# Kernel optimization log

Measured on AMD Instinct MI355X. Metric: run time of the kernel, lower is better.

## Reference

```python
import jax, jax.numpy as jnp
import numpy as np

TOP_K = 2

def setup_inputs() -> dict:
    key = jax.random.key(0)
    k0, k1, k2, k3, k4 = jax.random.split(key, 5)
    B, S, D, H, E = 2, 2048, 1024, 2048, 8
    x = jax.random.normal(k0, (B, S, D), dtype=jnp.float32)
    router_w = jax.random.normal(k1, (D, E), dtype=jnp.float32) * (1.0 / np.sqrt(D))
    wg = jax.random.normal(k2, (E, D, H), dtype=jnp.float32) * (1.0 / np.sqrt(D))
    wu = jax.random.normal(k3, (E, D, H), dtype=jnp.float32) * (1.0 / np.sqrt(D))
    wd = jax.random.normal(k4, (E, H, D), dtype=jnp.float32) * (1.0 / np.sqrt(H))
    return {"x": x, "router_w": router_w, "wg": wg, "wu": wu, "wd": wd}

def reference(x, router_w, wg, wu, wd):
    B, S, D = x.shape
    E = router_w.shape[1]
    xf = x.reshape(-1, D)                                   # [T, D]
    router_logits = xf @ router_w                           # [T, E]
    top_logits, top_idx = jax.lax.top_k(router_logits, TOP_K)
    top_w = jax.nn.softmax(top_logits, axis=-1)             # [T, k]
    # Dense combine weights: W[t, e] = routing weight if e in top-k of t, else 0.
    combine = jnp.sum(jax.nn.one_hot(top_idx, E, dtype=x.dtype) * top_w[..., None], axis=1)  # [T, E]
    # SwiGLU experts, computed for all tokens and masked by the combine weights
    # (mathematically identical to the gather/scatter form in the original).
    gate = jnp.einsum('td,edh->eth', xf, wg)                # [E, T, H]
    up = jnp.einsum('td,edh->eth', xf, wu)                  # [E, T, H]
    fused = jax.nn.silu(gate) * up                          # [E, T, H]
    expert_out = jnp.einsum('eth,ehd->etd', fused, wd)      # [E, T, D]
    y = jnp.einsum('etd,te->td', expert_out, combine)       # [T, D]
    return y.reshape(B, S, D)
```

## Files before the change

kernel.cpp:

```cpp
#include <hip/hip_runtime.h>
#include <hip/hip_bf16.h>

#define T_TOK 4096
#define DDIM  1024
#define HDIM  2048
#define NEXP  8
#define MAXSLOT 9216

typedef __attribute__((ext_vector_type(4))) float f32x4;
typedef __attribute__((ext_vector_type(8))) short s16x8;
typedef __hip_bfloat16 bf16;

typedef const void __attribute__((address_space(1))) gvoid;
typedef void __attribute__((address_space(3))) svoid;

__device__ __forceinline__ void gload16(const void* g, void* l) {
    __builtin_amdgcn_global_load_lds((gvoid*)g, (svoid*)l, 16, 0, 0);
}

__device__ __forceinline__ int frag_off(int rr, int kq) {
    int lr = rr >> 1;
    int ch = ((rr & 1) << 2) + (kq >> 3);
    return lr * 64 + (ch ^ (lr & 7)) * 8;
}

__global__ void router_cast_kernel(const float* __restrict__ x, const float* __restrict__ rw,
                                   int* __restrict__ r_e, float* __restrict__ r_w,
                                   bf16* __restrict__ xb) {
    int wave = threadIdx.x >> 6, lane = threadIdx.x & 63;
    int t = blockIdx.x * 4 + wave;
    const float* xr = x + (size_t)t * DDIM;
    bf16* xbr = xb + (size_t)t * DDIM;
    double acc[NEXP];
#pragma unroll
    for (int e = 0; e < NEXP; ++e) acc[e] = 0.0;
#pragma unroll
    for (int c = 0; c < 4; ++c) {
        int d = c * 256 + lane * 4;
        float4 v = *reinterpret_cast<const float4*>(xr + d);
        union { ushort4 u; bf16 h[4]; } o;
        o.h[0] = __float2bfloat16(v.x);
        o.h[1] = __float2bfloat16(v.y);
        o.h[2] = __float2bfloat16(v.z);
        o.h[3] = __float2bfloat16(v.w);
        *reinterpret_cast<ushort4*>(xbr + d) = o.u;
        const float* rw0 = rw + (size_t)d * NEXP;
#pragma unroll
        for (int j = 0; j < 4; ++j) {
            float xv = (&v.x)[j];
            const float* rwr = rw0 + j * NEXP;
#pragma unroll
            for (int e = 0; e < NEXP; ++e) acc[e] += (double)xv * (double)rwr[e];
        }
    }
#pragma unroll
    for (int e = 0; e < NEXP; ++e) {
#pragma unroll
        for (int off = 32; off > 0; off >>= 1) acc[e] += __shfl_down(acc[e], off);
    }
    if (lane == 0) {
        int i0 = 0; double v0 = acc[0];
#pragma unroll
        for (int e = 1; e < NEXP; ++e) if (acc[e] > v0) { v0 = acc[e]; i0 = e; }
        int i1 = -1; double v1 = -1e300;
#pragma unroll
        for (int e = 0; e < NEXP; ++e) { if (e == i0) continue; if (acc[e] > v1) { v1 = acc[e]; i1 = e; } }
        float w0 = 1.0f / (1.0f + expf((float)(v1 - v0)));
        float w1 = 1.0f - w0;
        r_e[2*t]   = i0; r_e[2*t+1] = i1;
        r_w[2*t]   = w0; r_w[2*t+1] = w1;
    }
}

__global__ void binning_kernel(const int* __restrict__ r_e, const float* __restrict__ r_w,
                               int* __restrict__ offs, int* __restrict__ cnt,
                               int* __restrict__ list, float* __restrict__ slot_w) {
    __shared__ int scnt[NEXP], scur[NEXP], soff[NEXP + 1];
    int tid = threadIdx.x;
    if (tid < NEXP) { scnt[tid] = 0; scur[tid] = 0; }
    __syncthreads();
    for (int i = tid; i < 2 * T_TOK; i += 512) atomicAdd(&scnt[r_e[i]], 1);
    __syncthreads();
    if (tid == 0) {
        int s = 0;
        for (int e = 0; e < NEXP; ++e) { soff[e] = s; s += (scnt[e] + 127) & ~127; }
        soff[NEXP] = s;
    }
    __syncthreads();
    if (tid < NEXP + 1) offs[tid] = soff[tid];
    if (tid < NEXP) cnt[tid] = scnt[tid];
    for (int i = tid; i < 2 * T_TOK; i += 512) {
        int e = r_e[i];
        int pos = atomicAdd(&scur[e], 1);
        int slot = soff[e] + pos;
        list[slot] = i >> 1;
        slot_w[slot] = r_w[i];
    }
}

__global__ void transpose_gu_kernel(const float* __restrict__ wg, const float* __restrict__ wu,
                                    bf16* __restrict__ wguT) {
    __shared__ bf16 tile[64][68];
    int which = blockIdx.z >> 3;
    int e = blockIdx.z & 7;
    const float* inp = (which ? wu : wg) + (size_t)e * DDIM * HDIM;
    bf16* outp = wguT + (size_t)e * 2 * HDIM * DDIM;
    int r0 = blockIdx.x * 64, c0 = blockIdx.y * 64;
    int tid = threadIdx.x;
#pragma unroll
    for (int i = 0; i < 4; ++i) {
        int idx = i * 256 + tid;
        int r = idx >> 4, c4 = (idx & 15) * 4;
        float4 v = *reinterpret_cast<const float4*>(inp + (size_t)(r0 + r) * HDIM + c0 + c4);
        union { ushort4 u; bf16 h[4]; } o;
        o.h[0] = __float2bfloat16(v.x);
        o.h[1] = __float2bfloat16(v.y);
        o.h[2] = __float2bfloat16(v.z);
        o.h[3] = __float2bfloat16(v.w);
        *reinterpret_cast<ushort4*>(&tile[r][c4]) = o.u;
    }
    __syncthreads();
#pragma unroll
    for (int i = 0; i < 4; ++i) {
        int idx = i * 256 + tid;
        int c = idx >> 4, r4 = (idx & 15) * 4;
        union { ushort4 u; bf16 h[4]; } w;
        w.h[0] = tile[r4 + 0][c];
        w.h[1] = tile[r4 + 1][c];
        w.h[2] = tile[r4 + 2][c];
        w.h[3] = tile[r4 + 3][c];
        *reinterpret_cast<ushort4*>(outp + ((size_t)(c0 + c) * 2 + which) * DDIM + r0 + r4) = w.u;
    }
}

__global__ void transpose_wd_kernel(const float* __restrict__ wd, bf16* __restrict__ wdT) {
    __shared__ bf16 tile[64][68];
    const float* inp = wd + (size_t)blockIdx.z * HDIM * DDIM;
    bf16* outp = wdT + (size_t)blockIdx.z * DDIM * HDIM;
    int r0 = blockIdx.x * 64, c0 = blockIdx.y * 64;
    int tid = threadIdx.x;
#pragma unroll
    for (int i = 0; i < 4; ++i) {
        int idx = i * 256 + tid;
        int r = idx >> 4, c4 = (idx & 15) * 4;
        float4 v = *reinterpret_cast<const float4*>(inp + (size_t)(r0 + r) * DDIM + c0 + c4);
        union { ushort4 u; bf16 h[4]; } o;
        o.h[0] = __float2bfloat16(v.x);
        o.h[1] = __float2bfloat16(v.y);
        o.h[2] = __float2bfloat16(v.z);
        o.h[3] = __float2bfloat16(v.w);
        *reinterpret_cast<ushort4*>(&tile[r][c4]) = o.u;
    }
    __syncthreads();
#pragma unroll
    for (int i = 0; i < 4; ++i) {
        int idx = i * 256 + tid;
        int c = idx >> 4, r4 = (idx & 15) * 4;
        union { ushort4 u; bf16 h[4]; } w;
        w.h[0] = tile[r4 + 0][c];
        w.h[1] = tile[r4 + 1][c];
        w.h[2] = tile[r4 + 2][c];
        w.h[3] = tile[r4 + 3][c];
        *reinterpret_cast<ushort4*>(outp + (size_t)(c0 + c) * HDIM + r0 + r4) = w.u;
    }
}

__device__ __forceinline__ int find_expert(const int* offs, int slot0) {
    int e = 0;
#pragma unroll
    for (int i = 0; i < NEXP - 1; ++i) e += (offs[e + 1] <= slot0) ? 1 : 0;
    return e;
}

__global__ __launch_bounds__(256, 2)
void gateup_kernel(const bf16* __restrict__ xb, const bf16* __restrict__ wguT,
                   const int* __restrict__ offs, const int* __restrict__ cnt,
                   const int* __restrict__ list, bf16* __restrict__ hbuf) {
    int slot0 = blockIdx.y * 128;
    if (slot0 >= offs[NEXP]) return;
    int e = find_expert(offs, slot0);
    int base = offs[e];
    int ne = cnt[e];
    int m0 = slot0 - base;
    int n0 = blockIdx.x * 128;

    __shared__ bf16 As[3][4096];
    __shared__ bf16 Bs[3][4096];

    int tid = threadIdx.x, lane = tid & 63, wid = tid >> 6;

    const bf16* bbase = wguT + (size_t)e * (2 * HDIM) * DDIM + (size_t)n0 * DDIM;

    const bf16* aS[2]; const bf16* bS[2];
    int sdst[2];
#pragma unroll
    for (int j = 0; j < 2; ++j) {
        int q = wid + j * 4;
        int lr = q * 8 + (lane >> 3);
        int ch = (lane & 7) ^ (lr & 7);
        int rr = 2 * lr + (ch >> 2);
        int koff = (ch & 3) * 8;
        int r = m0 + rr; if (r > ne - 1) r = ne - 1;
        aS[j] = xb + (size_t)list[base + r] * DDIM + koff;
        bS[j] = bbase + (size_t)rr * DDIM + koff;
        sdst[j] = q * 512;
    }

    int rl = lane & 15, kq = 8 * (lane >> 4);
    int wrow = (wid >> 1) * 64;
    int wcol = (wid & 1) * 64;
    int offA[4], offB[4];
#pragma unroll
    for (int mi = 0; mi < 4; ++mi) offA[mi] = frag_off(wrow + mi * 16 + rl, kq);
#pragma unroll
    for (int ni = 0; ni < 4; ++ni) offB[ni] = frag_off(wcol + ni * 16 + rl, kq);

    f32x4 zero4 = {0.f, 0.f, 0.f, 0.f};
    f32x4 acc[4][4];
#pragma unroll
    for (int mi = 0; mi < 4; ++mi)
#pragma unroll
        for (int ni = 0; ni < 4; ++ni) acc[mi][ni] = zero4;

    const int nk = DDIM / 32;

#define GU_STAGE(tt, buf)                                     \
    {                                                         \
        int k0 = (tt) * 32;                                   \
        gload16(aS[0] + k0, &As[buf][sdst[0]]);               \
        gload16(aS[1] + k0, &As[buf][sdst[1]]);               \
        gload16(bS[0] + k0, &Bs[buf][sdst[0]]);               \
        gload16(bS[1] + k0, &Bs[buf][sdst[1]]);               \
    }

    GU_STAGE(0, 0);
    GU_STAGE(1, 1);
    asm volatile("s_waitcnt vmcnt(4)" ::: "memory");
    __builtin_amdgcn_s_barrier();

    int cb = 0;
    for (int t = 0; t < nk; ++t) {
        int sb = cb + 2; if (sb >= 3) sb -= 3;
        if (t + 2 < nk) GU_STAGE(t + 2, sb);
        const bf16* Ab = As[cb];
        const bf16* Bb = Bs[cb];
        s16x8 a[4], b[4];
#pragma unroll
        for (int mi = 0; mi < 4; ++mi) a[mi] = *reinterpret_cast<const s16x8*>(Ab + offA[mi]);
#pragma unroll
        for (int ni = 0; ni < 4; ++ni) b[ni] = *reinterpret_cast<const s16x8*>(Bb + offB[ni]);
        __builtin_amdgcn_s_setprio(1);
#pragma unroll
        for (int mi = 0; mi < 4; ++mi)
#pragma unroll
            for (int ni = 0; ni < 4; ++ni)
                acc[mi][ni] = __builtin_amdgcn_mfma_f32_16x16x32_bf16(a[mi], b[ni], acc[mi][ni], 0, 0, 0);
        __builtin_amdgcn_s_setprio(0);
        __builtin_amdgcn_sched_barrier(0);
        if (t + 1 < nk) {
            if (t + 2 < nk) asm volatile("s_waitcnt vmcnt(4)" ::: "memory");
            else            asm volatile("s_waitcnt vmcnt(0)" ::: "memory");
            __builtin_amdgcn_s_barrier();
        }
        cb = cb + 1; if (cb >= 3) cb -= 3;
    }
#undef GU_STAGE

    int rbase = (lane >> 4) * 4, cbase = lane & 15;
    bool evenlane = (lane & 1) == 0;
#pragma unroll
    for (int mi = 0; mi < 4; ++mi) {
#pragma unroll
        for (int ni = 0; ni < 4; ++ni) {
#pragma unroll
            for (int r = 0; r < 4; ++r) {
                float own = acc[mi][ni][r];
                float oth = __shfl_xor(own, 1);
                int row = m0 + wrow + mi * 16 + rbase + r;
                if (evenlane && row < ne) {
                    float g = own, u = oth;
                    float h = (g / (1.0f + expf(-g))) * u;
                    int hcol = (n0 + wcol + ni * 16 + cbase) >> 1;
                    hbuf[(size_t)(base + row) * HDIM + hcol] = __float2bfloat16(h);
                }
            }
        }
    }
}

__global__ __launch_bounds__(256, 2)
void down_kernel(const bf16* __restrict__ hbuf, const bf16* __restrict__ wdT,
                 const int* __restrict__ offs, const int* __restrict__ cnt,
                 const int* __restrict__ list, const float* __restrict__ slot_w,
                 float* __restrict__ y) {
    int slot0 = blockIdx.y * 128;
    if (slot0 >= offs[NEXP]) return;
    int e = find_expert(offs, slot0);
    int base = offs[e];
    int ne = cnt[e];
    int m0 = slot0 - base;
    int n0 = blockIdx.x * 128;

    __shared__ bf16 As[3][4096];
    __shared__ bf16 Bs[3][4096];

    int tid = threadIdx.x, lane = tid & 63, wid = tid >> 6;

    const bf16* bbase = wdT + (size_t)e * DDIM * HDIM + (size_t)n0 * HDIM;

    const bf16* aS[2]; const bf16* bS[2];
    int sdst[2];
#pragma unroll
    for (int j = 0; j < 2; ++j) {
        int q = wid + j * 4;
        int lr = q * 8 + (lane >> 3);
        int ch = (lane & 7) ^ (lr & 7);
        int rr = 2 * lr + (ch >> 2);
        int koff = (ch & 3) * 8;
        int r = m0 + rr; if (r > ne - 1) r = ne - 1;
        aS[j] = hbuf + (size_t)(base + r) * HDIM + koff;
        bS[j] = bbase + (size_t)rr * HDIM + koff;
        sdst[j] = q * 512;
    }

    int rl = lane & 15, kq = 8 * (lane >> 4);
    int wrow = (wid >> 1) * 64;
    int wcol = (wid & 1) * 64;
    int offA[4], offB[4];
#pragma unroll
    for (int mi = 0; mi < 4; ++mi) offA[mi] = frag_off(wrow + mi * 16 + rl, kq);
#pragma unroll
    for (int ni = 0; ni < 4; ++ni) offB[ni] = frag_off(wcol + ni * 16 + rl, kq);

    f32x4 zero4 = {0.f, 0.f, 0.f, 0.f};
    f32x4 acc[4][4];
#pragma unroll
    for (int mi = 0; mi < 4; ++mi)
#pragma unroll
        for (int ni = 0; ni < 4; ++ni) acc[mi][ni] = zero4;

    const int nk = HDIM / 32;

#define DN_STAGE(tt, buf)                                     \
    {                                                         \
        int k0 = (tt) * 32;                                   \
        gload16(aS[0] + k0, &As[buf][sdst[0]]);               \
        gload16(aS[1] + k0, &As[buf][sdst[1]]);               \
        gload16(bS[0] + k0, &Bs[buf][sdst[0]]);               \
        gload16(bS[1] + k0, &Bs[buf][sdst[1]]);               \
    }

    DN_STAGE(0, 0);
    DN_STAGE(1, 1);
    asm volatile("s_waitcnt vmcnt(4)" ::: "memory");
    __builtin_amdgcn_s_barrier();

    int cb = 0;
    for (int t = 0; t < nk; ++t) {
        int sb = cb + 2; if (sb >= 3) sb -= 3;
        if (t + 2 < nk) DN_STAGE(t + 2, sb);
        const bf16* Ab = As[cb];
        const bf16* Bb = Bs[cb];
        s16x8 a[4], b[4];
#pragma unroll
        for (int mi = 0; mi < 4; ++mi) a[mi] = *reinterpret_cast<const s16x8*>(Ab + offA[mi]);
#pragma unroll
        for (int ni = 0; ni < 4; ++ni) b[ni] = *reinterpret_cast<const s16x8*>(Bb + offB[ni]);
        __builtin_amdgcn_s_setprio(1);
#pragma unroll
        for (int mi = 0; mi < 4; ++mi)
#pragma unroll
            for (int ni = 0; ni < 4; ++ni)
                acc[mi][ni] = __builtin_amdgcn_mfma_f32_16x16x32_bf16(a[mi], b[ni], acc[mi][ni], 0, 0, 0);
        __builtin_amdgcn_s_setprio(0);
        __builtin_amdgcn_sched_barrier(0);
        if (t + 1 < nk) {
            if (t + 2 < nk) asm volatile("s_waitcnt vmcnt(4)" ::: "memory");
            else            asm volatile("s_waitcnt vmcnt(0)" ::: "memory");
            __builtin_amdgcn_s_barrier();
        }
        cb = cb + 1; if (cb >= 3) cb -= 3;
    }
#undef DN_STAGE

    int rbase = (lane >> 4) * 4, cbase = lane & 15;
#pragma unroll
    for (int mi = 0; mi < 4; ++mi) {
#pragma unroll
        for (int r = 0; r < 4; ++r) {
            int row = m0 + wrow + mi * 16 + rbase + r;
            if (row < ne) {
                int slot = base + row;
                int tok = list[slot];
                float w = slot_w[slot];
                float* yrow = y + (size_t)tok * DDIM + n0 + wcol + cbase;
#pragma unroll
                for (int ni = 0; ni < 4; ++ni)
                    atomicAdd(yrow + ni * 16, w * acc[mi][ni][r]);
            }
        }
    }
}

extern "C" void kernel_launch(void* const* d_in, const int* in_sizes, int n_in,
                              void* d_out, int out_size, void* d_ws, size_t ws_size,
                              hipStream_t stream) {
    const float* x  = (const float*)d_in[0];
    const float* rw = (const float*)d_in[1];
    const float* wg = (const float*)d_in[2];
    const float* wu = (const float*)d_in[3];
    const float* wd = (const float*)d_in[4];
    float* y = (float*)d_out;

    char* ws = (char*)d_ws;
    int*   r_e    = (int*)  (ws + 0);
    float* r_w    = (float*)(ws + 32768);
    int*   offs   = (int*)  (ws + 65600);
    int*   cnt    = (int*)  (ws + 65640);
    int*   list   = (int*)  (ws + 65792);
    float* slot_w = (float*)(ws + 65792 + 4 * MAXSLOT);
    bf16*  xb     = (bf16*) (ws + 1048576ull);
    bf16*  wguT   = (bf16*) (ws + 16777216ull);
    bf16*  wdT    = (bf16*) (ws + 83886080ull);
    bf16*  hbuf   = (bf16*) (ws + 117440512ull);

    transpose_gu_kernel<<<dim3(DDIM / 64, HDIM / 64, 2 * NEXP), 256, 0, stream>>>(wg, wu, wguT);
    transpose_wd_kernel<<<dim3(HDIM / 64, DDIM / 64, NEXP), 256, 0, stream>>>(wd, wdT);

    router_cast_kernel<<<dim3(T_TOK / 4), 256, 0, stream>>>(x, rw, r_e, r_w, xb);
    binning_kernel<<<dim3(1), 512, 0, stream>>>(r_e, r_w, offs, cnt, list, slot_w);

    hipMemsetAsync(d_out, 0, (size_t)out_size * sizeof(float), stream);

    gateup_kernel<<<dim3(2 * HDIM / 128, MAXSLOT / 128, 1), 256, 0, stream>>>(
        xb, wguT, offs, cnt, list, hbuf);
    down_kernel<<<dim3(DDIM / 128, MAXSLOT / 128, 1), 256, 0, stream>>>(
        hbuf, wdT, offs, cnt, list, slot_w, y);
}
```

Baseline: 286.2 us.

## Widen GEMM tiles to 128x256 with 512 threads and double buffering

Both grouped GEMM kernels move from 128x128 tiles with 4 waves to 128x256 tiles with 8 waves per block. Each A tile is now reused across twice as many output columns, and the block count along N is halved. The three-stage LDS pipeline is cut to two stages with a full vmcnt(0) wait every iteration, so each global load has less time to hide behind compute. LDS per block stays about the same at 48KB.

Measured after the change: 288.8 us. Within noise of the previous version (+0.9%).

```diff
diff --git a/kernel.cpp b/kernel.cpp
--- a/kernel.cpp
+++ b/kernel.cpp
@@ -172,7 +172,7 @@
     return e;
 }
 
-__global__ __launch_bounds__(256, 2)
+__global__ __launch_bounds__(512, 2)
 void gateup_kernel(const bf16* __restrict__ xb, const bf16* __restrict__ wguT,
                    const int* __restrict__ offs, const int* __restrict__ cnt,
                    const int* __restrict__ list, bf16* __restrict__ hbuf) {
@@ -182,33 +182,41 @@
     int base = offs[e];
     int ne = cnt[e];
     int m0 = slot0 - base;
-    int n0 = blockIdx.x * 128;
-
-    __shared__ bf16 As[3][4096];
-    __shared__ bf16 Bs[3][4096];
+    int n0 = blockIdx.x * 256;
+
+    __shared__ bf16 As[2][4096];
+    __shared__ bf16 Bs[2][8192];
 
     int tid = threadIdx.x, lane = tid & 63, wid = tid >> 6;
 
     const bf16* bbase = wguT + (size_t)e * (2 * HDIM) * DDIM + (size_t)n0 * DDIM;
 
-    const bf16* aS[2]; const bf16* bS[2];
-    int sdst[2];
-#pragma unroll
-    for (int j = 0; j < 2; ++j) {
-        int q = wid + j * 4;
+    const bf16* aS; const bf16* bS[2];
+    int sdstA, sdstB[2];
+    {
+        int q = wid;
         int lr = q * 8 + (lane >> 3);
         int ch = (lane & 7) ^ (lr & 7);
         int rr = 2 * lr + (ch >> 2);
         int koff = (ch & 3) * 8;
         int r = m0 + rr; if (r > ne - 1) r = ne - 1;
-        aS[j] = xb + (size_t)list[base + r] * DDIM + koff;
+        aS = xb + (size_t)list[base + r] * DDIM + koff;
+        sdstA = q * 512;
+    }
+#pragma unroll
+    for (int j = 0; j < 2; ++j) {
+        int q = wid + j * 8;
+        int lr = q * 8 + (lane >> 3);
+        int ch = (lane & 7) ^ (lr & 7);
+        int rr = 2 * lr + (ch >> 2);
+        int koff = (ch & 3) * 8;
         bS[j] = bbase + (size_t)rr * DDIM + koff;
-        sdst[j] = q * 512;
+        sdstB[j] = q * 512;
     }
 
     int rl = lane & 15, kq = 8 * (lane >> 4);
-    int wrow = (wid >> 1) * 64;
-    int wcol = (wid & 1) * 64;
+    int wrow = (wid >> 2) * 64;
+    int wcol = (wid & 3) * 64;
     int offA[4], offB[4];
 #pragma unroll
     for (int mi = 0; mi < 4; ++mi) offA[mi] = frag_off(wrow + mi * 16 + rl, kq);
@@ -227,23 +235,20 @@
 #define GU_STAGE(tt, buf)                                     \
     {                                                         \
         int k0 = (tt) * 32;                                   \
-        gload16(aS[0] + k0, &As[buf][sdst[0]]);               \
-        gload16(aS[1] + k0, &As[buf][sdst[1]]);               \
-        gload16(bS[0] + k0, &Bs[buf][sdst[0]]);               \
-        gload16(bS[1] + k0, &Bs[buf][sdst[1]]);               \
+        gload16(aS + k0, &As[buf][sdstA]);                    \
+        gload16(bS[0] + k0, &Bs[buf][sdstB[0]]);              \
+        gload16(bS[1] + k0, &Bs[buf][sdstB[1]]);              \
     }
 
     GU_STAGE(0, 0);
-    GU_STAGE(1, 1);
-    asm volatile("s_waitcnt vmcnt(4)" ::: "memory");
+    asm volatile("s_waitcnt vmcnt(0)" ::: "memory");
     __builtin_amdgcn_s_barrier();
 
-    int cb = 0;
+    int cur = 0;
     for (int t = 0; t < nk; ++t) {
-        int sb = cb + 2; if (sb >= 3) sb -= 3;
-        if (t + 2 < nk) GU_STAGE(t + 2, sb);
-        const bf16* Ab = As[cb];
-        const bf16* Bb = Bs[cb];
+        if (t + 1 < nk) GU_STAGE(t + 1, cur ^ 1);
+        const bf16* Ab = As[cur];
+        const bf16* Bb = Bs[cur];
         s16x8 a[4], b[4];
 #pragma unroll
         for (int mi = 0; mi < 4; ++mi) a[mi] = *reinterpret_cast<const s16x8*>(Ab + offA[mi]);
@@ -258,11 +263,10 @@
         __builtin_amdgcn_s_setprio(0);
         __builtin_amdgcn_sched_barrier(0);
         if (t + 1 < nk) {
-            if (t + 2 < nk) asm volatile("s_waitcnt vmcnt(4)" ::: "memory");
-            else            asm volatile("s_waitcnt vmcnt(0)" ::: "memory");
+            asm volatile("s_waitcnt vmcnt(0)" ::: "memory");
             __builtin_amdgcn_s_barrier();
         }
-        cb = cb + 1; if (cb >= 3) cb -= 3;
+        cur ^= 1;
     }
 #undef GU_STAGE
 
@@ -288,7 +292,7 @@
     }
 }
 
-__global__ __launch_bounds__(256, 2)
+__global__ __launch_bounds__(512, 2)
 void down_kernel(const bf16* __restrict__ hbuf, const bf16* __restrict__ wdT,
                  const int* __restrict__ offs, const int* __restrict__ cnt,
                  const int* __restrict__ list, const float* __restrict__ slot_w,
@@ -299,33 +303,41 @@
     int base = offs[e];
     int ne = cnt[e];
     int m0 = slot0 - base;
-    int n0 = blockIdx.x * 128;
-
-    __shared__ bf16 As[3][4096];
-    __shared__ bf16 Bs[3][4096];
+    int n0 = blockIdx.x * 256;
+
+    __shared__ bf16 As[2][4096];
+    __shared__ bf16 Bs[2][8192];
 
     int tid = threadIdx.x, lane = tid & 63, wid = tid >> 6;
 
     const bf16* bbase = wdT + (size_t)e * DDIM * HDIM + (size_t)n0 * HDIM;
 
-    const bf16* aS[2]; const bf16* bS[2];
-    int sdst[2];
-#pragma unroll
-    for (int j = 0; j < 2; ++j) {
-        int q = wid + j * 4;
+    const bf16* aS; const bf16* bS[2];
+    int sdstA, sdstB[2];
+    {
+        int q = wid;
         int lr = q * 8 + (lane >> 3);
         int ch = (lane & 7) ^ (lr & 7);
         int rr = 2 * lr + (ch >> 2);
         int koff = (ch & 3) * 8;
         int r = m0 + rr; if (r > ne - 1) r = ne - 1;
-        aS[j] = hbuf + (size_t)(base + r) * HDIM + koff;
+        aS = hbuf + (size_t)(base + r) * HDIM + koff;
+        sdstA = q * 512;
+    }
+#pragma unroll
+    for (int j = 0; j < 2; ++j) {
+        int q = wid + j * 8;
+        int lr = q * 8 + (lane >> 3);
+        int ch = (lane & 7) ^ (lr & 7);
+        int rr = 2 * lr + (ch >> 2);
+        int koff = (ch & 3) * 8;
         bS[j] = bbase + (size_t)rr * HDIM + koff;
-        sdst[j] = q * 512;
+        sdstB[j] = q * 512;
     }
 
     int rl = lane & 15, kq = 8 * (lane >> 4);
-    int wrow = (wid >> 1) * 64;
-    int wcol = (wid & 1) * 64;
+    int wrow = (wid >> 2) * 64;
+    int wcol = (wid & 3) * 64;
     int offA[4], offB[4];
 #pragma unroll
     for (int mi = 0; mi < 4; ++mi) offA[mi] = frag_off(wrow + mi * 16 + rl, kq);
@@ -344,23 +356,20 @@
 #define DN_STAGE(tt, buf)                                     \
     {                                                         \
         int k0 = (tt) * 32;                                   \
-        gload16(aS[0] + k0, &As[buf][sdst[0]]);               \
-        gload16(aS[1] + k0, &As[buf][sdst[1]]);               \
-        gload16(bS[0] + k0, &Bs[buf][sdst[0]]);               \
-        gload16(bS[1] + k0, &Bs[buf][sdst[1]]);               \
+        gload16(aS + k0, &As[buf][sdstA]);                    \
+        gload16(bS[0] + k0, &Bs[buf][sdstB[0]]);              \
+        gload16(bS[1] + k0, &Bs[buf][sdstB[1]]);              \
     }
 
     DN_STAGE(0, 0);
-    DN_STAGE(1, 1);
-    asm volatile("s_waitcnt vmcnt(4)" ::: "memory");
+    asm volatile("s_waitcnt vmcnt(0)" ::: "memory");
     __builtin_amdgcn_s_barrier();
 
-    int cb = 0;
+    int cur = 0;
     for (int t = 0; t < nk; ++t) {
-        int sb = cb + 2; if (sb >= 3) sb -= 3;
-        if (t + 2 < nk) DN_STAGE(t + 2, sb);
-        const bf16* Ab = As[cb];
-        const bf16* Bb = Bs[cb];
+        if (t + 1 < nk) DN_STAGE(t + 1, cur ^ 1);
+        const bf16* Ab = As[cur];
+        const bf16* Bb = Bs[cur];
         s16x8 a[4], b[4];
 #pragma unroll
         for (int mi = 0; mi < 4; ++mi) a[mi] = *reinterpret_cast<const s16x8*>(Ab + offA[mi]);
@@ -375,11 +384,10 @@
         __builtin_amdgcn_s_setprio(0);
         __builtin_amdgcn_sched_barrier(0);
         if (t + 1 < nk) {
-            if (t + 2 < nk) asm volatile("s_waitcnt vmcnt(4)" ::: "memory");
-            else            asm volatile("s_waitcnt vmcnt(0)" ::: "memory");
+            asm volatile("s_waitcnt vmcnt(0)" ::: "memory");
             __builtin_amdgcn_s_barrier();
         }
-        cb = cb + 1; if (cb >= 3) cb -= 3;
+        cur ^= 1;
     }
 #undef DN_STAGE
 
@@ -432,8 +440,8 @@
 
     hipMemsetAsync(d_out, 0, (size_t)out_size * sizeof(float), stream);
 
-    gateup_kernel<<<dim3(2 * HDIM / 128, MAXSLOT / 128, 1), 256, 0, stream>>>(
+    gateup_kernel<<<dim3(2 * HDIM / 256, MAXSLOT / 128, 1), 512, 0, stream>>>(
         xb, wguT, offs, cnt, list, hbuf);
-    down_kernel<<<dim3(DDIM / 128, MAXSLOT / 128, 1), 256, 0, stream>>>(
+    down_kernel<<<dim3(DDIM / 256, MAXSLOT / 128, 1), 512, 0, stream>>>(
         hbuf, wdT, offs, cnt, list, slot_w, y);
 }
```

## Use 512-thread blocks with BK=64 double-buffered tiles in expert GEMMs

Applied to the files above, without the earlier changes.

Both the gate/up and down expert GEMM kernels move from 256 threads with a 3-stage BK=32 pipeline to 512 threads (8 waves, each owning a 64x32 sub-tile) with a 2-stage BK=64 double buffer. The LDS layout becomes a simple 64-wide row with XOR swizzle, and the number of k-iterations and barriers per tile is halved. The aim is more waves to hide latency and less loop and sync overhead per k-step. In exchange, each wave does half the MFMAs per fragment load, so it gets less register reuse, and prefetch depth drops to one stage with an extra barrier per iteration.

Result: no change. 284.1 us (-0.7%).

```diff
diff --git a/kernel.cpp b/kernel.cpp
--- a/kernel.cpp
+++ b/kernel.cpp
@@ -16,12 +16,6 @@
 
 __device__ __forceinline__ void gload16(const void* g, void* l) {
     __builtin_amdgcn_global_load_lds((gvoid*)g, (svoid*)l, 16, 0, 0);
-}
-
-__device__ __forceinline__ int frag_off(int rr, int kq) {
-    int lr = rr >> 1;
-    int ch = ((rr & 1) << 2) + (kq >> 3);
-    return lr * 64 + (ch ^ (lr & 7)) * 8;
 }
 
 __global__ void router_cast_kernel(const float* __restrict__ x, const float* __restrict__ rw,
@@ -172,7 +166,7 @@
     return e;
 }
 
-__global__ __launch_bounds__(256, 2)
+__global__ __launch_bounds__(512, 2)
 void gateup_kernel(const bf16* __restrict__ xb, const bf16* __restrict__ wguT,
                    const int* __restrict__ offs, const int* __restrict__ cnt,
                    const int* __restrict__ list, bf16* __restrict__ hbuf) {
@@ -184,10 +178,12 @@
     int m0 = slot0 - base;
     int n0 = blockIdx.x * 128;
 
-    __shared__ bf16 As[3][4096];
-    __shared__ bf16 Bs[3][4096];
+    __shared__ bf16 As[2][8192];
+    __shared__ bf16 Bs[2][8192];
 
     int tid = threadIdx.x, lane = tid & 63, wid = tid >> 6;
+    int sub = lane >> 3;
+    int koff = 8 * ((lane & 7) ^ sub);
 
     const bf16* bbase = wguT + (size_t)e * (2 * HDIM) * DDIM + (size_t)n0 * DDIM;
 
@@ -195,75 +191,68 @@
     int sdst[2];
 #pragma unroll
     for (int j = 0; j < 2; ++j) {
-        int q = wid + j * 4;
-        int lr = q * 8 + (lane >> 3);
-        int ch = (lane & 7) ^ (lr & 7);
-        int rr = 2 * lr + (ch >> 2);
-        int koff = (ch & 3) * 8;
-        int r = m0 + rr; if (r > ne - 1) r = ne - 1;
+        int q = wid + j * 8;
+        int row = q * 8 + sub;
+        int r = m0 + row; if (r > ne - 1) r = ne - 1;
         aS[j] = xb + (size_t)list[base + r] * DDIM + koff;
-        bS[j] = bbase + (size_t)rr * DDIM + koff;
+        bS[j] = bbase + (size_t)row * DDIM + koff;
         sdst[j] = q * 512;
     }
 
     int rl = lane & 15, kq = 8 * (lane >> 4);
-    int wrow = (wid >> 1) * 64;
-    int wcol = (wid & 1) * 64;
-    int offA[4], offB[4];
-#pragma unroll
-    for (int mi = 0; mi < 4; ++mi) offA[mi] = frag_off(wrow + mi * 16 + rl, kq);
-#pragma unroll
-    for (int ni = 0; ni < 4; ++ni) offB[ni] = frag_off(wcol + ni * 16 + rl, kq);
+    int wrow = (wid >> 2) * 64;
+    int wcol = (wid & 3) * 32;
+    int xorv = (rl & 7) * 8;
 
     f32x4 zero4 = {0.f, 0.f, 0.f, 0.f};
-    f32x4 acc[4][4];
-#pragma unroll
-    for (int mi = 0; mi < 4; ++mi)
-#pragma unroll
-        for (int ni = 0; ni < 4; ++ni) acc[mi][ni] = zero4;
-
-    const int nk = DDIM / 32;
+    f32x4 acc[4][2];
+#pragma unroll
+    for (int mi = 0; mi < 4; ++mi) { acc[mi][0] = zero4; acc[mi][1] = zero4; }
+
+    const int nk = DDIM / 64;
 
 #define GU_STAGE(tt, buf)                                     \
     {                                                         \
-        int k0 = (tt) * 32;                                   \
+        int k0 = (tt) * 64;                                   \
         gload16(aS[0] + k0, &As[buf][sdst[0]]);               \
         gload16(aS[1] + k0, &As[buf][sdst[1]]);               \
         gload16(bS[0] + k0, &Bs[buf][sdst[0]]);               \
         gload16(bS[1] + k0, &Bs[buf][sdst[1]]);               \
     }
 
+#define GU_COMPUTE(Ab, Bb)                                                        \
+    _Pragma("unroll")                                                             \
+    for (int kk = 0; kk < 2; ++kk) {                                              \
+        int kos = (kk * 32 + kq) ^ xorv;                                          \
+        s16x8 a[4], b[2];                                                         \
+        _Pragma("unroll")                                                         \
+        for (int mi = 0; mi < 4; ++mi)                                            \
+            a[mi] = *reinterpret_cast<const s16x8*>(&(Ab)[(wrow + mi * 16 + rl) * 64 + kos]); \
+        _Pragma("unroll")                                                         \
+        for (int ni = 0; ni < 2; ++ni)                                            \
+            b[ni] = *reinterpret_cast<const s16x8*>(&(Bb)[(wcol + ni * 16 + rl) * 64 + kos]); \
+        __builtin_amdgcn_s_setprio(1);                                            \
+        _Pragma("unroll")                                                         \
+        for (int mi = 0; mi < 4; ++mi)                                            \
+            _Pragma("unroll")                                                     \
+            for (int ni = 0; ni < 2; ++ni)                                        \
+                acc[mi][ni] = __builtin_amdgcn_mfma_f32_16x16x32_bf16(a[mi], b[ni], acc[mi][ni], 0, 0, 0); \
+        __builtin_amdgcn_s_setprio(0);                                            \
+    }
+
     GU_STAGE(0, 0);
     GU_STAGE(1, 1);
-    asm volatile("s_waitcnt vmcnt(4)" ::: "memory");
-    __builtin_amdgcn_s_barrier();
-
-    int cb = 0;
+
     for (int t = 0; t < nk; ++t) {
-        int sb = cb + 2; if (sb >= 3) sb -= 3;
-        if (t + 2 < nk) GU_STAGE(t + 2, sb);
-        const bf16* Ab = As[cb];
-        const bf16* Bb = Bs[cb];
-        s16x8 a[4], b[4];
-#pragma unroll
-        for (int mi = 0; mi < 4; ++mi) a[mi] = *reinterpret_cast<const s16x8*>(Ab + offA[mi]);
-#pragma unroll
-        for (int ni = 0; ni < 4; ++ni) b[ni] = *reinterpret_cast<const s16x8*>(Bb + offB[ni]);
-        __builtin_amdgcn_s_setprio(1);
-#pragma unroll
-        for (int mi = 0; mi < 4; ++mi)
-#pragma unroll
-            for (int ni = 0; ni < 4; ++ni)
-                acc[mi][ni] = __builtin_amdgcn_mfma_f32_16x16x32_bf16(a[mi], b[ni], acc[mi][ni], 0, 0, 0);
-        __builtin_amdgcn_s_setprio(0);
+        if (t + 1 < nk) asm volatile("s_waitcnt vmcnt(4)" ::: "memory");
+        else            asm volatile("s_waitcnt vmcnt(0)" ::: "memory");
+        __builtin_amdgcn_s_barrier();
+        GU_COMPUTE(As[t & 1], Bs[t & 1]);
         __builtin_amdgcn_sched_barrier(0);
-        if (t + 1 < nk) {
-            if (t + 2 < nk) asm volatile("s_waitcnt vmcnt(4)" ::: "memory");
-            else            asm volatile("s_waitcnt vmcnt(0)" ::: "memory");
-            __builtin_amdgcn_s_barrier();
-        }
-        cb = cb + 1; if (cb >= 3) cb -= 3;
-    }
+        __builtin_amdgcn_s_barrier();
+        if (t + 2 < nk) GU_STAGE(t + 2, t & 1);
+    }
+#undef GU_COMPUTE
 #undef GU_STAGE
 
     int rbase = (lane >> 4) * 4, cbase = lane & 15;
@@ -271,7 +260,7 @@
 #pragma unroll
     for (int mi = 0; mi < 4; ++mi) {
 #pragma unroll
-        for (int ni = 0; ni < 4; ++ni) {
+        for (int ni = 0; ni < 2; ++ni) {
 #pragma unroll
             for (int r = 0; r < 4; ++r) {
                 float own = acc[mi][ni][r];
@@ -288,7 +277,7 @@
     }
 }
 
-__global__ __launch_bounds__(256, 2)
+__global__ __launch_bounds__(512, 2)
 void down_kernel(const bf16* __restrict__ hbuf, const bf16* __restrict__ wdT,
                  const int* __restrict__ offs, const int* __restrict__ cnt,
                  const int* __restrict__ list, const float* __restrict__ slot_w,
@@ -301,10 +290,12 @@
     int m0 = slot0 - base;
     int n0 = blockIdx.x * 128;
 
-    __shared__ bf16 As[3][4096];
-    __shared__ bf16 Bs[3][4096];
+    __shared__ bf16 As[2][8192];
+    __shared__ bf16 Bs[2][8192];
 
     int tid = threadIdx.x, lane = tid & 63, wid = tid >> 6;
+    int sub = lane >> 3;
+    int koff = 8 * ((lane & 7) ^ sub);
 
     const bf16* bbase = wdT + (size_t)e * DDIM * HDIM + (size_t)n0 * HDIM;
 
@@ -312,75 +303,68 @@
     int sdst[2];
 #pragma unroll
     for (int j = 0; j < 2; ++j) {
-        int q = wid + j * 4;
-        int lr = q * 8 + (lane >> 3);
-        int ch = (lane & 7) ^ (lr & 7);
-        int rr = 2 * lr + (ch >> 2);
-        int koff = (ch & 3) * 8;
-        int r = m0 + rr; if (r > ne - 1) r = ne - 1;
+        int q = wid + j * 8;
+        int row = q * 8 + sub;
+        int r = m0 + row; if (r > ne - 1) r = ne - 1;
         aS[j] = hbuf + (size_t)(base + r) * HDIM + koff;
-        bS[j] = bbase + (size_t)rr * HDIM + koff;
+        bS[j] = bbase + (size_t)row * HDIM + koff;
         sdst[j] = q * 512;
     }
 
     int rl = lane & 15, kq = 8 * (lane >> 4);
-    int wrow = (wid >> 1) * 64;
-    int wcol = (wid & 1) * 64;
-    int offA[4], offB[4];
-#pragma unroll
-    for (int mi = 0; mi < 4; ++mi) offA[mi] = frag_off(wrow + mi * 16 + rl, kq);
-#pragma unroll
-    for (int ni = 0; ni < 4; ++ni) offB[ni] = frag_off(wcol + ni * 16 + rl, kq);
+    int wrow = (wid >> 2) * 64;
+    int wcol = (wid & 3) * 32;
+    int xorv = (rl & 7) * 8;
 
     f32x4 zero4 = {0.f, 0.f, 0.f, 0.f};
-    f32x4 acc[4][4];
-#pragma unroll
-    for (int mi = 0; mi < 4; ++mi)
-#pragma unroll
-        for (int ni = 0; ni < 4; ++ni) acc[mi][ni] = zero4;
-
-    const int nk = HDIM / 32;
+    f32x4 acc[4][2];
+#pragma unroll
+    for (int mi = 0; mi < 4; ++mi) { acc[mi][0] = zero4; acc[mi][1] = zero4; }
+
+    const int nk = HDIM / 64;
 
 #define DN_STAGE(tt, buf)                                     \
     {                                                         \
-        int k0 = (tt) * 32;                                   \
+        int k0 = (tt) * 64;                                   \
         gload16(aS[0] + k0, &As[buf][sdst[0]]);               \
         gload16(aS[1] + k0, &As[buf][sdst[1]]);               \
         gload16(bS[0] + k0, &Bs[buf][sdst[0]]);               \
         gload16(bS[1] + k0, &Bs[buf][sdst[1]]);               \
     }
 
+#define DN_COMPUTE(Ab, Bb)                                                        \
+    _Pragma("unroll")                                                             \
+    for (int kk = 0; kk < 2; ++kk) {                                              \
+        int kos = (kk * 32 + kq) ^ xorv;                                          \
+        s16x8 a[4], b[2];                                                         \
+        _Pragma("unroll")                                                         \
+        for (int mi = 0; mi < 4; ++mi)                                            \
+            a[mi] = *reinterpret_cast<const s16x8*>(&(Ab)[(wrow + mi * 16 + rl) * 64 + kos]); \
+        _Pragma("unroll")                                                         \
+        for (int ni = 0; ni < 2; ++ni)                                            \
+            b[ni] = *reinterpret_cast<const s16x8*>(&(Bb)[(wcol + ni * 16 + rl) * 64 + kos]); \
+        __builtin_amdgcn_s_setprio(1);                                            \
+        _Pragma("unroll")                                                         \
+        for (int mi = 0; mi < 4; ++mi)                                            \
+            _Pragma("unroll")                                                     \
+            for (int ni = 0; ni < 2; ++ni)                                        \
+                acc[mi][ni] = __builtin_amdgcn_mfma_f32_16x16x32_bf16(a[mi], b[ni], acc[mi][ni], 0, 0, 0); \
+        __builtin_amdgcn_s_setprio(0);                                            \
+    }
+
     DN_STAGE(0, 0);
     DN_STAGE(1, 1);
-    asm volatile("s_waitcnt vmcnt(4)" ::: "memory");
-    __builtin_amdgcn_s_barrier();
-
-    int cb = 0;
+
     for (int t = 0; t < nk; ++t) {
-        int sb = cb + 2; if (sb >= 3) sb -= 3;
-        if (t + 2 < nk) DN_STAGE(t + 2, sb);
-        const bf16* Ab = As[cb];
-        const bf16* Bb = Bs[cb];
-        s16x8 a[4], b[4];
-#pragma unroll
-        for (int mi = 0; mi < 4; ++mi) a[mi] = *reinterpret_cast<const s16x8*>(Ab + offA[mi]);
-#pragma unroll
-        for (int ni = 0; ni < 4; ++ni) b[ni] = *reinterpret_cast<const s16x8*>(Bb + offB[ni]);
-        __builtin_amdgcn_s_setprio(1);
-#pragma unroll
-        for (int mi = 0; mi < 4; ++mi)
-#pragma unroll
-            for (int ni = 0; ni < 4; ++ni)
-                acc[mi][ni] = __builtin_amdgcn_mfma_f32_16x16x32_bf16(a[mi], b[ni], acc[mi][ni], 0, 0, 0);
-        __builtin_amdgcn_s_setprio(0);
+        if (t + 1 < nk) asm volatile("s_waitcnt vmcnt(4)" ::: "memory");
+        else            asm volatile("s_waitcnt vmcnt(0)" ::: "memory");
+        __builtin_amdgcn_s_barrier();
+        DN_COMPUTE(As[t & 1], Bs[t & 1]);
         __builtin_amdgcn_sched_barrier(0);
-        if (t + 1 < nk) {
-            if (t + 2 < nk) asm volatile("s_waitcnt vmcnt(4)" ::: "memory");
-            else            asm volatile("s_waitcnt vmcnt(0)" ::: "memory");
-            __builtin_amdgcn_s_barrier();
-        }
-        cb = cb + 1; if (cb >= 3) cb -= 3;
-    }
+        __builtin_amdgcn_s_barrier();
+        if (t + 2 < nk) DN_STAGE(t + 2, t & 1);
+    }
+#undef DN_COMPUTE
 #undef DN_STAGE
 
     int rbase = (lane >> 4) * 4, cbase = lane & 15;
@@ -395,7 +379,7 @@
                 float w = slot_w[slot];
                 float* yrow = y + (size_t)tok * DDIM + n0 + wcol + cbase;
 #pragma unroll
-                for (int ni = 0; ni < 4; ++ni)
+                for (int ni = 0; ni < 2; ++ni)
                     atomicAdd(yrow + ni * 16, w * acc[mi][ni][r]);
             }
         }
@@ -432,8 +416,8 @@
 
     hipMemsetAsync(d_out, 0, (size_t)out_size * sizeof(float), stream);
 
-    gateup_kernel<<<dim3(2 * HDIM / 128, MAXSLOT / 128, 1), 256, 0, stream>>>(
+    gateup_kernel<<<dim3(2 * HDIM / 128, MAXSLOT / 128, 1), 512, 0, stream>>>(
         xb, wguT, offs, cnt, list, hbuf);
-    down_kernel<<<dim3(DDIM / 128, MAXSLOT / 128, 1), 256, 0, stream>>>(
+    down_kernel<<<dim3(DDIM / 128, MAXSLOT / 128, 1), 512, 0, stream>>>(
         hbuf, wdT, offs, cnt, list, slot_w, y);
 }
```
